# Kernel tuning notes

Hardware: AMD Instinct MI355X
Metric: run time of the kernel (lower is better)

Reference implementation:

```python
import jax, jax.numpy as jnp
import numpy as np

EMBED = 1024
HEADS = 16
HEAD_SIZE = EMBED // HEADS


def setup_inputs() -> dict:
    key = jax.random.key(0)
    kx, kk, kq, kv, kp, kb = jax.random.split(key, 6)
    s = 1.0 / np.sqrt(EMBED)
    return {
        "x": jax.random.normal(kx, (4, 2048, EMBED), dtype=jnp.float32),
        "Wk": jax.random.uniform(kk, (EMBED, EMBED), jnp.float32, -s, s),
        "Wq": jax.random.uniform(kq, (EMBED, EMBED), jnp.float32, -s, s),
        "Wv": jax.random.uniform(kv, (EMBED, EMBED), jnp.float32, -s, s),
        "Wp": jax.random.uniform(kp, (EMBED, EMBED), jnp.float32, -s, s),
        "bp": jax.random.uniform(kb, (EMBED,), jnp.float32, -s, s),
    }


def reference(x, Wk, Wq, Wv, Wp, bp):
    B, T, C = x.shape
    H, D = HEADS, HEAD_SIZE
    # torch nn.Linear: y = x @ W.T
    k = (x @ Wk.T).reshape(B, T, H, D).transpose(0, 2, 1, 3)  # [B,H,T,D]
    q = (x @ Wq.T).reshape(B, T, H, D).transpose(0, 2, 1, 3)
    v = (x @ Wv.T).reshape(B, T, H, D).transpose(0, 2, 1, 3)
    att = jnp.einsum('bhqd,bhkd->bhqk', q, k) * (1.0 / np.sqrt(D))
    causal = jnp.tril(jnp.ones((T, T), dtype=bool))
    att = jnp.where(causal, att, -jnp.inf)
    att = jax.nn.softmax(att, axis=-1)
    # dropout is identity in eval mode
    out = jnp.einsum('bhqk,bhkd->bhqd', att, v)
    out = out.transpose(0, 2, 1, 3).reshape(B, T, C)
    return out @ Wp.T + bp
```

## Files before the change

### kernel.cpp

```cpp
#include <hip/hip_runtime.h>
#include <hip/hip_bf16.h>

typedef __attribute__((ext_vector_type(8))) short bf16x8;
typedef __attribute__((ext_vector_type(4))) float f32x4;

#define DEVINL __device__ __forceinline__

static DEVINL ushort f2b(float f) {
    union { float f; unsigned int u; } v; v.f = f;
    unsigned int u = v.u;
    unsigned int r = (u + 0x7FFFu + ((u >> 16) & 1u)) >> 16;
    return (ushort)r;
}

static DEVINL unsigned int cvtpk(float lo, float hi) {
    unsigned int r;
    asm("v_cvt_pk_bf16_f32 %0, %1, %2" : "=v"(r) : "v"(lo), "v"(hi));
    return r;
}

static DEVINL int swz(int row, int c) {
    return row * 64 + (((c ^ (row & 7)) & 7) << 3);
}

__global__ void cast_w_kernel(const float* __restrict__ Wq, const float* __restrict__ Wk,
                              const float* __restrict__ Wv, const float* __restrict__ Wp,
                              ushort* __restrict__ out) {
    int idx = blockIdx.x * blockDim.x + threadIdx.x;
    int col4 = idx & 255;
    int row  = idx >> 8;
    int which = row >> 10;
    int r = row & 1023;
    const float* src = (which == 0) ? Wq : (which == 1) ? Wk : (which == 2) ? Wv : Wp;
    float s = (which == 0) ? 0.125f : 1.0f;
    float4 v = ((const float4*)src)[r * 256 + col4];
    ushort4 o;
    o.x = f2b(v.x * s); o.y = f2b(v.y * s); o.z = f2b(v.z * s); o.w = f2b(v.w * s);
    ((ushort4*)out)[idx] = o;
}

__global__ void cast_x_kernel(const float* __restrict__ x, ushort* __restrict__ out) {
    int idx = blockIdx.x * blockDim.x + threadIdx.x;
    float4 v = ((const float4*)x)[idx];
    ushort4 o;
    o.x = f2b(v.x); o.y = f2b(v.y); o.z = f2b(v.z); o.w = f2b(v.w);
    ((ushort4*)out)[idx] = o;
}

template<bool BF16_OUT>
__global__ __launch_bounds__(256) void gemm_bt_kernel(const ushort* __restrict__ A,
                                                      const ushort* __restrict__ B,
                                                      void* __restrict__ Cv,
                                                      const float* __restrict__ bias,
                                                      int M, int N, int K) {
    __shared__ ushort Al[128][72];
    __shared__ ushort Bl[128][72];
    const int tid = threadIdx.x;
    const int m0 = blockIdx.y * 128, n0 = blockIdx.x * 128;
    const int lane = tid & 63, wid = tid >> 6;
    const int wm = (wid >> 1) * 64, wn = (wid & 1) * 64;
    const int lr = lane & 15, lg = lane >> 4;

    f32x4 acc[4][4];
    #pragma unroll
    for (int i = 0; i < 4; ++i)
        #pragma unroll
        for (int j = 0; j < 4; ++j)
            acc[i][j] = (f32x4){0.f, 0.f, 0.f, 0.f};

    const int arow = tid >> 3;
    const int ac8  = (tid & 7) * 8;
    const int nkt = K >> 6;
    for (int kt = 0; kt < nkt; ++kt) {
        __syncthreads();
        #pragma unroll
        for (int i = 0; i < 4; ++i) {
            int row = arow + i * 32;
            *(uint4*)&Al[row][ac8] = *(const uint4*)&A[(size_t)(m0 + row) * K + kt * 64 + ac8];
            *(uint4*)&Bl[row][ac8] = *(const uint4*)&B[(size_t)(n0 + row) * K + kt * 64 + ac8];
        }
        __syncthreads();
        #pragma unroll
        for (int kk = 0; kk < 64; kk += 32) {
            bf16x8 af[4], bfr[4];
            #pragma unroll
            for (int mi = 0; mi < 4; ++mi)
                af[mi] = *(const bf16x8*)&Al[wm + mi * 16 + lr][kk + lg * 8];
            #pragma unroll
            for (int ni = 0; ni < 4; ++ni)
                bfr[ni] = *(const bf16x8*)&Bl[wn + ni * 16 + lr][kk + lg * 8];
            #pragma unroll
            for (int mi = 0; mi < 4; ++mi)
                #pragma unroll
                for (int ni = 0; ni < 4; ++ni)
                    acc[mi][ni] = __builtin_amdgcn_mfma_f32_16x16x32_bf16(af[mi], bfr[ni], acc[mi][ni], 0, 0, 0);
        }
    }
    #pragma unroll
    for (int mi = 0; mi < 4; ++mi) {
        #pragma unroll
        for (int r = 0; r < 4; ++r) {
            int gm = m0 + wm + mi * 16 + lg * 4 + r;
            #pragma unroll
            for (int ni = 0; ni < 4; ++ni) {
                int gn = n0 + wn + ni * 16 + lr;
                float val = acc[mi][ni][r];
                if (BF16_OUT) {
                    ((ushort*)Cv)[(size_t)gm * N + gn] = f2b(val);
                } else {
                    ((float*)Cv)[(size_t)gm * N + gn] = val + bias[gn];
                }
            }
        }
    }
}

__global__ void transpose_v_kernel(const ushort* __restrict__ QKV, ushort* __restrict__ Vt) {
    __shared__ ushort tile[32][33];
    int t0 = blockIdx.x * 32;
    int n0 = blockIdx.y * 32;
    int tx = threadIdx.x, ty = threadIdx.y;
    #pragma unroll
    for (int i = 0; i < 4; ++i) {
        int row = ty + i * 8;
        tile[row][tx] = QKV[(size_t)(t0 + row) * 3072 + 2048 + n0 + tx];
    }
    __syncthreads();
    #pragma unroll
    for (int i = 0; i < 4; ++i) {
        int row = ty + i * 8;
        Vt[(size_t)(n0 + row) * 8192 + t0 + tx] = tile[tx][row];
    }
}

__global__ __launch_bounds__(256, 3) void attn_kernel(const ushort* __restrict__ QKV,
                                                      const ushort* __restrict__ Vt,
                                                      ushort* __restrict__ O) {
    __shared__ ushort Kl[2][64 * 64];
    __shared__ ushort Vl[2][64 * 64];
    __shared__ ushort Pl[4][32 * 64];

    const int bh = blockIdx.x, b = bh >> 4, h = bh & 15;
    const int qb = (int)gridDim.y - 1 - (int)blockIdx.y;
    const int q0 = qb * 128;
    const int tid = threadIdx.x, lane = tid & 63, w = tid >> 6;
    const int lr = lane & 15, lg = lane >> 4;
    const int qw = q0 + w * 32;

    bf16x8 qf[2][2];
    {
        const ushort* qp = QKV + (size_t)(b * 2048 + qw + lr) * 3072 + h * 64 + lg * 8;
        qf[0][0] = *(const bf16x8*)qp;
        qf[0][1] = *(const bf16x8*)(qp + 32);
        qf[1][0] = *(const bf16x8*)(qp + (size_t)16 * 3072);
        qf[1][1] = *(const bf16x8*)(qp + (size_t)16 * 3072 + 32);
    }

    f32x4 o[4][2];
    #pragma unroll
    for (int di = 0; di < 4; ++di)
        #pragma unroll
        for (int nt_ = 0; nt_ < 2; ++nt_)
            o[di][nt_] = (f32x4){0.f, 0.f, 0.f, 0.f};
    float mrow[2] = {-INFINITY, -INFINITY};
    float lrow[2] = {0.f, 0.f};

    const size_t kbase = (size_t)(b * 2048) * 3072 + 1024 + h * 64;
    const size_t vbase = (size_t)(h * 64) * 8192 + (size_t)b * 2048;
    const int srow = tid >> 2, sc = tid & 3;
    const int ss0 = swz(srow, sc), ss1 = swz(srow, sc + 4);
    char* const pw = (char*)&Pl[w][0];

    const int nt = qb * 2 + 2;
    uint4 kr0, kr1, vr0, vr1;

    #define LOADT(t) do {                                                      \
        const int kv0s = (t) * 64;                                             \
        const ushort* kg = QKV + kbase + (size_t)(kv0s + srow) * 3072;         \
        const ushort* vg = Vt + vbase + (size_t)srow * 8192 + kv0s;            \
        kr0 = *(const uint4*)&kg[sc * 8];                                      \
        kr1 = *(const uint4*)&kg[sc * 8 + 32];                                 \
        vr0 = *(const uint4*)&vg[sc * 8];                                      \
        vr1 = *(const uint4*)&vg[sc * 8 + 32];                                 \
    } while (0)

    #define WRITET(bufi) do {                                                  \
        *(uint4*)&Kl[bufi][ss0] = kr0;                                         \
        *(uint4*)&Kl[bufi][ss1] = kr1;                                         \
        *(uint4*)&Vl[bufi][ss0] = vr0;                                         \
        *(uint4*)&Vl[bufi][ss1] = vr1;                                         \
    } while (0)

    LOADT(0);
    WRITET(0);
    __syncthreads();

    for (int t = 0; t < nt; ++t) {
        const int buf = t & 1;
        const int kv0 = t * 64;
        const bool have_next = (t + 1 < nt);
        if (have_next) LOADT(t + 1);

        if (kv0 <= qw + 31) {
            f32x4 s[4][2];
            #pragma unroll
            for (int mi = 0; mi < 4; ++mi)
                #pragma unroll
                for (int nt_ = 0; nt_ < 2; ++nt_)
                    s[mi][nt_] = (f32x4){0.f, 0.f, 0.f, 0.f};
            __builtin_amdgcn_s_setprio(1);
            #pragma unroll
            for (int ks = 0; ks < 2; ++ks) {
                #pragma unroll
                for (int mi = 0; mi < 4; ++mi) {
                    bf16x8 kf = *(const bf16x8*)&Kl[buf][swz(mi * 16 + lr, ks * 4 + lg)];
                    s[mi][0] = __builtin_amdgcn_mfma_f32_16x16x32_bf16(kf, qf[0][ks], s[mi][0], 0, 0, 0);
                    s[mi][1] = __builtin_amdgcn_mfma_f32_16x16x32_bf16(kf, qf[1][ks], s[mi][1], 0, 0, 0);
                }
            }
            __builtin_amdgcn_s_setprio(0);

            #pragma unroll
            for (int nt_ = 0; nt_ < 2; ++nt_) {
                const int qn = qw + nt_ * 16 + lr;
                const bool full = (kv0 + 63 <= qw + nt_ * 16);
                const int kvb = kv0 + lg * 4;
                float v[4][4];
                #pragma unroll
                for (int mi = 0; mi < 4; ++mi)
                    #pragma unroll
                    for (int r = 0; r < 4; ++r) {
                        float x = s[mi][nt_][r];
                        if (!full) x = (kvb + mi * 16 + r <= qn) ? x : -INFINITY;
                        v[mi][r] = x;
                    }
                float mx0 = fmaxf(fmaxf(v[0][0], v[0][1]), fmaxf(v[0][2], v[0][3]));
                float mx1 = fmaxf(fmaxf(v[1][0], v[1][1]), fmaxf(v[1][2], v[1][3]));
                float mx2 = fmaxf(fmaxf(v[2][0], v[2][1]), fmaxf(v[2][2], v[2][3]));
                float mx3 = fmaxf(fmaxf(v[3][0], v[3][1]), fmaxf(v[3][2], v[3][3]));
                float pmax = fmaxf(fmaxf(mx0, mx1), fmaxf(mx2, mx3));
                pmax = fmaxf(pmax, __shfl_xor(pmax, 16));
                pmax = fmaxf(pmax, __shfl_xor(pmax, 32));

                const bool defer = __all(pmax <= mrow[nt_] + 8.0f);
                float mn;
                if (defer) {
                    mn = mrow[nt_];
                } else {
                    mn = fmaxf(mrow[nt_], pmax);
                    const float al = __expf(mrow[nt_] - mn);
                    lrow[nt_] *= al;
                    #pragma unroll
                    for (int di = 0; di < 4; ++di)
                        #pragma unroll
                        for (int r = 0; r < 4; ++r)
                            o[di][nt_][r] *= al;
                    mrow[nt_] = mn;
                }
                float p[4][4];
                #pragma unroll
                for (int mi = 0; mi < 4; ++mi)
                    #pragma unroll
                    for (int r = 0; r < 4; ++r)
                        p[mi][r] = __expf(v[mi][r] - mn);
                float rs = ((p[0][0] + p[0][1]) + (p[0][2] + p[0][3]))
                         + ((p[1][0] + p[1][1]) + (p[1][2] + p[1][3]))
                         + ((p[2][0] + p[2][1]) + (p[2][2] + p[2][3]))
                         + ((p[3][0] + p[3][1]) + (p[3][2] + p[3][3]));
                rs += __shfl_xor(rs, 16);
                rs += __shfl_xor(rs, 32);
                lrow[nt_] += rs;

                const int rowoff = (nt_ * 16 + lr) * 128;
                const int xr = (lr & 7) << 4;
                #pragma unroll
                for (int mi = 0; mi < 4; ++mi) {
                    uint2 val;
                    val.x = cvtpk(p[mi][0], p[mi][1]);
                    val.y = cvtpk(p[mi][2], p[mi][3]);
                    *(uint2*)(pw + rowoff + ((32 * mi + 8 * lg) ^ xr)) = val;
                }
            }
            asm volatile("s_waitcnt lgkmcnt(0)" ::: "memory");
            __builtin_amdgcn_sched_barrier(0);

            __builtin_amdgcn_s_setprio(1);
            #pragma unroll
            for (int ks = 0; ks < 2; ++ks) {
                bf16x8 pb[2];
                #pragma unroll
                for (int nt_ = 0; nt_ < 2; ++nt_) {
                    const int byteoff = (nt_ * 16 + lr) * 128 + (((64 * ks + 16 * lg)) ^ ((lr & 7) << 4));
                    pb[nt_] = *(const bf16x8*)(pw + byteoff);
                }
                #pragma unroll
                for (int di = 0; di < 4; ++di) {
                    bf16x8 vf = *(const bf16x8*)&Vl[buf][swz(di * 16 + lr, ks * 4 + lg)];
                    o[di][0] = __builtin_amdgcn_mfma_f32_16x16x32_bf16(vf, pb[0], o[di][0], 0, 0, 0);
                    o[di][1] = __builtin_amdgcn_mfma_f32_16x16x32_bf16(vf, pb[1], o[di][1], 0, 0, 0);
                }
            }
            __builtin_amdgcn_s_setprio(0);
        }
        if (have_next) WRITET(buf ^ 1);
        __syncthreads();
    }
    #undef LOADT
    #undef WRITET

    #pragma unroll
    for (int nt_ = 0; nt_ < 2; ++nt_) {
        const float inv = 1.0f / lrow[nt_];
        const int rowoff = (nt_ * 16 + lr) * 128;
        const int xr = (lr & 7) << 4;
        #pragma unroll
        for (int di = 0; di < 4; ++di) {
            uint2 val;
            val.x = cvtpk(o[di][nt_][0] * inv, o[di][nt_][1] * inv);
            val.y = cvtpk(o[di][nt_][2] * inv, o[di][nt_][3] * inv);
            *(uint2*)(pw + rowoff + ((32 * di + 8 * lg) ^ xr)) = val;
        }
    }
    asm volatile("s_waitcnt lgkmcnt(0)" ::: "memory");
    __builtin_amdgcn_sched_barrier(0);
    {
        const int row = lane >> 1;
        const int half = lane & 1;
        const int xr2 = (row & 7) << 4;
        ushort* og = O + (size_t)(b * 2048 + qw + row) * 1024 + h * 64 + half * 32;
        #pragma unroll
        for (int c = 0; c < 4; ++c) {
            uint4 val = *(const uint4*)(pw + row * 128 + ((half * 64 + c * 16) ^ xr2));
            *(uint4*)&og[c * 8] = val;
        }
    }
}

extern "C" void kernel_launch(void* const* d_in, const int* in_sizes, int n_in,
                              void* d_out, int out_size, void* d_ws, size_t ws_size,
                              hipStream_t stream) {
    const float* x  = (const float*)d_in[0];
    const float* Wk = (const float*)d_in[1];
    const float* Wq = (const float*)d_in[2];
    const float* Wv = (const float*)d_in[3];
    const float* Wp = (const float*)d_in[4];
    const float* bp = (const float*)d_in[5];
    float* out = (float*)d_out;

    char* ws = (char*)d_ws;
    ushort* Xb   = (ushort*)(ws);
    ushort* Wcat = (ushort*)(ws + 16777216);
    ushort* QKV  = (ushort*)(ws + 25165824);
    ushort* Vt   = (ushort*)(ws + 75497472);
    ushort* Obuf = (ushort*)(ws + 92274688);

    cast_w_kernel<<<4096, 256, 0, stream>>>(Wq, Wk, Wv, Wp, Wcat);
    cast_x_kernel<<<8192, 256, 0, stream>>>(x, Xb);
    gemm_bt_kernel<true><<<dim3(24, 64), 256, 0, stream>>>(Xb, Wcat, QKV, nullptr, 8192, 3072, 1024);
    transpose_v_kernel<<<dim3(256, 32), dim3(32, 8), 0, stream>>>(QKV, Vt);
    attn_kernel<<<dim3(64, 16), 256, 0, stream>>>(QKV, Vt, Obuf);
    gemm_bt_kernel<false><<<dim3(8, 64), 256, 0, stream>>>(Obuf, Wcat + (size_t)3072 * 1024, out, bp, 8192, 1024, 1024);
}
```

Before: 189.4 us.

## Use direct global-to-LDS loads and XCD-aware block remapping in GEMM

The GEMM tile loads now use global_load_lds, which writes global memory straight into shared memory and bypasses registers. The LDS tiles become unpadded 128x64 arrays. Block IDs are remapped to a 1D grid so that consecutive tiles land on the same XCD for better L2 reuse. The unpadded layout risks LDS bank conflicts on fragment reads.

```diff
diff --git a/kernel.cpp b/kernel.cpp
--- a/kernel.cpp
+++ b/kernel.cpp
@@ -17,6 +17,13 @@
     unsigned int r;
     asm("v_cvt_pk_bf16_f32 %0, %1, %2" : "=v"(r) : "v"(lo), "v"(hi));
     return r;
+}
+
+static DEVINL void gload_lds16(const ushort* g, ushort* l) {
+    __builtin_amdgcn_global_load_lds(
+        (const __attribute__((address_space(1))) unsigned int*)g,
+        (__attribute__((address_space(3))) unsigned int*)l,
+        16, 0, 0);
 }
 
 static DEVINL int swz(int row, int c) {
@@ -52,11 +59,18 @@
                                                       const ushort* __restrict__ B,
                                                       void* __restrict__ Cv,
                                                       const float* __restrict__ bias,
-                                                      int M, int N, int K) {
-    __shared__ ushort Al[128][72];
-    __shared__ ushort Bl[128][72];
+                                                      int M, int N, int K, int gx) {
+    __shared__ ushort Al[128 * 64];
+    __shared__ ushort Bl[128 * 64];
     const int tid = threadIdx.x;
-    const int m0 = blockIdx.y * 128, n0 = blockIdx.x * 128;
+
+    const int nwg = (int)gridDim.x;
+    const int cpx = nwg >> 3;
+    const int orig = (int)blockIdx.x;
+    const int wgid = (orig & 7) * cpx + (orig >> 3);
+    const int bx = wgid % gx, by = wgid / gx;
+    const int m0 = by * 128, n0 = bx * 128;
+
     const int lane = tid & 63, wid = tid >> 6;
     const int wm = (wid >> 1) * 64, wn = (wid & 1) * 64;
     const int lr = lane & 15, lg = lane >> 4;
@@ -68,16 +82,21 @@
         for (int j = 0; j < 4; ++j)
             acc[i][j] = (f32x4){0.f, 0.f, 0.f, 0.f};
 
-    const int arow = tid >> 3;
-    const int ac8  = (tid & 7) * 8;
+    const int grow = wid * 32 + (lane >> 3);
+    const int gcol = (lane & 7) * 8;
+    const ushort* ga = A + (size_t)(m0 + grow) * K + gcol;
+    const ushort* gb = B + (size_t)(n0 + grow) * K + gcol;
+    ushort* la = &Al[wid * 32 * 64];
+    ushort* lb = &Bl[wid * 32 * 64];
+
     const int nkt = K >> 6;
     for (int kt = 0; kt < nkt; ++kt) {
+        const int kof = kt * 64;
         __syncthreads();
         #pragma unroll
-        for (int i = 0; i < 4; ++i) {
-            int row = arow + i * 32;
-            *(uint4*)&Al[row][ac8] = *(const uint4*)&A[(size_t)(m0 + row) * K + kt * 64 + ac8];
-            *(uint4*)&Bl[row][ac8] = *(const uint4*)&B[(size_t)(n0 + row) * K + kt * 64 + ac8];
+        for (int j = 0; j < 4; ++j) {
+            gload_lds16(ga + (size_t)(j * 8) * K + kof, la + j * 8 * 64);
+            gload_lds16(gb + (size_t)(j * 8) * K + kof, lb + j * 8 * 64);
         }
         __syncthreads();
         #pragma unroll
@@ -85,10 +104,10 @@
             bf16x8 af[4], bfr[4];
             #pragma unroll
             for (int mi = 0; mi < 4; ++mi)
-                af[mi] = *(const bf16x8*)&Al[wm + mi * 16 + lr][kk + lg * 8];
+                af[mi] = *(const bf16x8*)&Al[(wm + mi * 16 + lr) * 64 + kk + lg * 8];
             #pragma unroll
             for (int ni = 0; ni < 4; ++ni)
-                bfr[ni] = *(const bf16x8*)&Bl[wn + ni * 16 + lr][kk + lg * 8];
+                bfr[ni] = *(const bf16x8*)&Bl[(wn + ni * 16 + lr) * 64 + kk + lg * 8];
             #pragma unroll
             for (int mi = 0; mi < 4; ++mi)
                 #pragma unroll
@@ -356,8 +375,8 @@
 
     cast_w_kernel<<<4096, 256, 0, stream>>>(Wq, Wk, Wv, Wp, Wcat);
     cast_x_kernel<<<8192, 256, 0, stream>>>(x, Xb);
-    gemm_bt_kernel<true><<<dim3(24, 64), 256, 0, stream>>>(Xb, Wcat, QKV, nullptr, 8192, 3072, 1024);
+    gemm_bt_kernel<true><<<1536, 256, 0, stream>>>(Xb, Wcat, QKV, nullptr, 8192, 3072, 1024, 24);
     transpose_v_kernel<<<dim3(256, 32), dim3(32, 8), 0, stream>>>(QKV, Vt);
     attn_kernel<<<dim3(64, 16), 256, 0, stream>>>(QKV, Vt, Obuf);
-    gemm_bt_kernel<false><<<dim3(8, 64), 256, 0, stream>>>(Obuf, Wcat + (size_t)3072 * 1024, out, bp, 8192, 1024, 1024);
-}
+    gemm_bt_kernel<false><<<512, 256, 0, stream>>>(Obuf, Wcat + (size_t)3072 * 1024, out, bp, 8192, 1024, 1024, 8);
+}
```

Result: slower. 205.1 us (+8.3%).
